# Kernel optimization log

Hardware: AMD Instinct MI355X
Metric: run time of the kernel (lower is better)

Reference implementation:

```python
import jax, jax.numpy as jnp
import numpy as np

AH, AW = 8, 8            # aligned_height, aligned_width
SCALE = 0.0625           # spatial_scale = 1/16
IMG = 1024               # image size implied by 64x64 feature map at stride 16


def setup_inputs() -> dict:
    key = jax.random.key(0)
    k1, k2, k3, k4, k5 = jax.random.split(key, 5)
    B, C, H, W = 4, 256, 64, 64
    N = 2000
    features = jax.random.normal(k1, (B, C, H, W), dtype=jnp.float32)
    # ROIs: (batch_idx, x1, y1, x2, y2) in image coordinates
    bidx = jax.random.randint(k2, (N,), 0, B).astype(jnp.float32)
    cx = jax.random.uniform(k3, (N,), minval=0.0, maxval=IMG)
    cy = jax.random.uniform(k4, (N,), minval=0.0, maxval=IMG)
    wh = jax.random.uniform(k5, (N, 2), minval=32.0, maxval=512.0)
    x1 = jnp.clip(cx - wh[:, 0] / 2, 0.0, IMG - 1.0)
    y1 = jnp.clip(cy - wh[:, 1] / 2, 0.0, IMG - 1.0)
    x2 = jnp.clip(cx + wh[:, 0] / 2, x1 + 16.0, float(IMG))
    y2 = jnp.clip(cy + wh[:, 1] / 2, y1 + 16.0, float(IMG))
    rois = jnp.stack([bidx, x1, y1, x2, y2], axis=1).astype(jnp.float32)
    return {"features": features, "rois": rois}


def _roi_align(features, rois):
    # Classic RoIAlign (crop_and_resize style): one bilinear sample per output
    # cell, sample grid spans the ROI with (aligned-1) intervals.
    B, C, H, W = features.shape
    N = rois.shape[0]
    b = rois[:, 0].astype(jnp.int32)
    x1 = rois[:, 1] * SCALE
    y1 = rois[:, 2] * SCALE
    x2 = rois[:, 3] * SCALE
    y2 = rois[:, 4] * SCALE
    bin_h = (y2 - y1) / (AH - 1.0)
    bin_w = (x2 - x1) / (AW - 1.0)
    ys = y1[:, None, None] + bin_h[:, None, None] * jnp.arange(AH, dtype=jnp.float32)[None, :, None]
    xs = x1[:, None, None] + bin_w[:, None, None] * jnp.arange(AW, dtype=jnp.float32)[None, None, :]
    ys = jnp.broadcast_to(ys, (N, AH, AW))
    xs = jnp.broadcast_to(xs, (N, AH, AW))
    valid = (ys >= 0) & (ys < H) & (xs >= 0) & (xs < W)
    y0 = jnp.floor(ys)
    x0 = jnp.floor(xs)
    ly = ys - y0  # bilinear weights
    lx = xs - x0
    iy0 = jnp.clip(y0.astype(jnp.int32), 0, H - 1)
    ix0 = jnp.clip(x0.astype(jnp.int32), 0, W - 1)
    iy1 = jnp.clip(iy0 + 1, 0, H - 1)
    ix1 = jnp.clip(ix0 + 1, 0, W - 1)
    bb = b[:, None, None]

    def g(iy, ix):
        return features[bb, :, iy, ix]  # [N, AH, AW, C]

    ly_ = ly[..., None]
    lx_ = lx[..., None]
    v = ((1 - ly_) * (1 - lx_) * g(iy0, ix0)
         + (1 - ly_) * lx_ * g(iy0, ix1)
         + ly_ * (1 - lx_) * g(iy1, ix0)
         + ly_ * lx_ * g(iy1, ix1))
    v = jnp.where(valid[..., None], v, 0.0)
    return jnp.transpose(v, (0, 3, 1, 2))  # [N, C, AH, AW]


def _max_pool_2x2_s1(x):
    # max_pool2d(kernel_size=2, stride=1): [N,C,h,w] -> [N,C,h-1,w-1]
    return jnp.maximum(
        jnp.maximum(x[:, :, :-1, :-1], x[:, :, :-1, 1:]),
        jnp.maximum(x[:, :, 1:, :-1], x[:, :, 1:, 1:]),
    )


def reference(features, rois):
    x = _roi_align(features, rois)
    return _max_pool_2x2_s1(x)  # [N, C, AH-1, AW-1]
```

## Files before the change

kernel.cpp:

```cpp
#include <hip/hip_runtime.h>
#include <cstdint>

constexpr int CCH = 256;
constexpr int HH  = 64;
constexpr int WW  = 64;
constexpr int OHW = 49;
constexpr float RSCALE = 0.0625f;

#define FMUL __fmul_rn
#define FADD __fadd_rn
#define FSUB __fsub_rn
#define FDIV __fdiv_rn

typedef float     v4f __attribute__((ext_vector_type(4)));
typedef _Float16  h2  __attribute__((ext_vector_type(2)));
typedef _Float16  h4  __attribute__((ext_vector_type(4)));

__device__ __forceinline__ h2 pkrtz(float a, float b) {
  auto t = __builtin_amdgcn_cvt_pkrtz(a, b);
  union { decltype(t) s; h2 d; } c; c.s = t; return c.d;
}
__device__ __forceinline__ h4 bcast4(float a) {
  h2 t = pkrtz(a, a);
  return __builtin_shufflevector(t, t, 0, 1, 0, 1);
}
__device__ __forceinline__ h4 u2h(uint2 u) {
  union { uint2 u; h4 h; } c; c.u = u; return c.h;
}
__device__ __forceinline__ h4 h4max(h4 a, h4 b) {
  return __builtin_elementwise_max(a, b);
}

__global__ __launch_bounds__(256) void ktrans_sched(const float* __restrict__ in,
                                                    unsigned short* __restrict__ out,
                                                    const float* __restrict__ rois,
                                                    int N, int slots, int do_sched,
                                                    int B, int* __restrict__ meta) {
  const int t = threadIdx.x;

  if ((int)blockIdx.z == B) {
    if (blockIdx.x != 0 || blockIdx.y != 0 || !do_sched) return;
    __shared__ int cnt[4], rnk[4], off[4], slack[4], excess[4];
    if (t < 4) { cnt[t] = 0; rnk[t] = 0; }
    __syncthreads();
    for (int i = t; i < N; i += 256) atomicAdd(&cnt[(int)rois[i * 5]], 1);
    __syncthreads();
    if (t == 0) {
      int o = 0, cs = 0, ce = 0;
      for (int p = 0; p < 4; ++p) {
        off[p] = o; o += cnt[p];
        slack[p]  = cs; if (slots - cnt[p] > 0) cs += slots - cnt[p];
        excess[p] = ce; if (cnt[p] - slots > 0) ce += cnt[p] - slots;
        meta[p] = cnt[p]; meta[4 + p] = off[p]; meta[8 + p] = slack[p];
      }
    }
    __syncthreads();
    int* perm = meta + 16;
    for (int i = t; i < N; i += 256) {
      const int b = (int)rois[i * 5];
      perm[off[b] + atomicAdd(&rnk[b], 1)] = i;
    }
    __syncthreads();
    int* extra = meta + 16 + N;
    for (int p = 0; p < 4; ++p) {
      const int ex = cnt[p] - slots;
      for (int e = t; e < ex; e += 256) extra[excess[p] + e] = perm[off[p] + slots + e];
    }
    return;
  }

  __shared__ float tile[64][65];
  const int b  = blockIdx.z;
  const int c0 = blockIdx.y * 64;
  const int s0 = blockIdx.x * 64;
  const float* inb = in + (size_t)b * CCH * (HH * WW);
  unsigned short* outb = out + (size_t)b * (HH * WW) * CCH;

  const int cl = t >> 4, sq = t & 15;
#pragma unroll
  for (int k = 0; k < 4; ++k) {
    const int c = cl + 16 * k;
    const v4f v = __builtin_nontemporal_load(
        (const v4f*)(inb + (size_t)(c0 + c) * (HH * WW) + s0 + 4 * sq));
    tile[c][4 * sq + 0] = v[0];
    tile[c][4 * sq + 1] = v[1];
    tile[c][4 * sq + 2] = v[2];
    tile[c][4 * sq + 3] = v[3];
  }
  __syncthreads();
  const int cq = t & 15, rl = t >> 4;
#pragma unroll
  for (int k = 0; k < 4; ++k) {
    const int r = rl + 16 * k;
    union { h2 h; unsigned u; } p0, p1;
    p0.h.x = (_Float16)tile[4 * cq + 0][r];
    p0.h.y = (_Float16)tile[4 * cq + 1][r];
    p1.h.x = (_Float16)tile[4 * cq + 2][r];
    p1.h.y = (_Float16)tile[4 * cq + 3][r];
    uint2 w; w.x = p0.u; w.y = p1.u;
    *(uint2*)(outb + (size_t)(s0 + r) * CCH + c0 + 4 * cq) = w;
  }
}

__global__ __launch_bounds__(256, 6) void roi_kernel11(const uint2* __restrict__ feat,
                                                       const float* __restrict__ rois,
                                                       const int* __restrict__ meta,
                                                       int N, int use_perm,
                                                       float* __restrict__ out) {
  __shared__ __attribute__((aligned(16))) h4       ldsA[OHW * 32];
  __shared__ __attribute__((aligned(16))) _Float16 ldsC[(CCH / 2) * OHW];
  const int i = blockIdx.x;
  const int t = threadIdx.x;
  const int g = t & 31;
  const int r = t >> 5;

  int n, half;
  if (use_perm) {
    const int p = (i & 7) >> 1;
    half        = i & 1;
    const int s = i >> 3;
    const int c_ = meta[p];
    const int o_ = meta[4 + p];
    const int sl = meta[8 + p];
    const int* perm  = meta + 16;
    const int* extra = meta + 16 + N;
    n = (s < c_) ? perm[o_ + s] : extra[sl + (s - c_)];
  } else {
    n = i >> 1; half = i & 1;
  }

  const float rb = rois[n * 5 + 0];
  const float x1 = FMUL(rois[n * 5 + 1], RSCALE);
  const float y1 = FMUL(rois[n * 5 + 2], RSCALE);
  const float x2 = FMUL(rois[n * 5 + 3], RSCALE);
  const float y2 = FMUL(rois[n * 5 + 4], RSCALE);
  const int   b  = (int)rb;
  const float bh = FDIV(FSUB(y2, y1), 7.0f);
  const float bw = FDIV(FSUB(x2, x1), 7.0f);

  int   xo0[8], xo1[8];
  float lx[8];
  bool  xv[8];
#pragma unroll
  for (int q = 0; q < 8; ++q) {
    const float xs = FADD(x1, FMUL(bw, (float)q));
    xv[q] = (xs >= 0.0f) && (xs < (float)WW);
    const float xf = floorf(xs);
    lx[q] = FSUB(xs, xf);
    int a = (int)xf;
    a = a < 0 ? 0 : (a > WW - 1 ? WW - 1 : a);
    xo0[q] = a * (CCH / 4);
    xo1[q] = ((a + 1 > WW - 1) ? WW - 1 : a + 1) * (CCH / 4);
  }

  const float ys = FADD(y1, FMUL(bh, (float)r));
  const bool  yv = (ys >= 0.0f) && (ys < (float)HH);
  const float yf = floorf(ys);
  const float ly = FSUB(ys, yf);
  int d = (int)yf;
  d = d < 0 ? 0 : (d > HH - 1 ? HH - 1 : d);
  const int d1 = (d + 1 > HH - 1) ? HH - 1 : d + 1;

  const uint2* fb = feat + (size_t)b * (HH * WW) * (CCH / 4) + (half * 32 + g);
  const uint2* r0 = fb + (size_t)d  * (WW * (CCH / 4));
  const uint2* r1 = fb + (size_t)d1 * (WW * (CCH / 4));
  const float wy1 = ly, wy0 = 1.0f - ly;

  h4 hc[7], vprev;
#pragma unroll
  for (int h = 0; h < 2; ++h) {
    uint2 g00[4], g01[4], g10[4], g11[4];
#pragma unroll
    for (int q = 0; q < 4; ++q) {
      const int s = 4 * h + q;
      g00[q] = r0[xo0[s]];
      g01[q] = r0[xo1[s]];
      g10[q] = r1[xo0[s]];
      g11[q] = r1[xo1[s]];
    }
    h4 v[4];
#pragma unroll
    for (int q = 0; q < 4; ++q) {
      const int s = 4 * h + q;
      const bool ok = yv && xv[s];
      const float wx1 = lx[s], wx0 = 1.0f - wx1;
      const h4 w00 = bcast4(wy0 * wx0);
      const h4 w01 = bcast4(wy0 * wx1);
      const h4 w10 = bcast4(wy1 * wx0);
      const h4 w11 = bcast4(wy1 * wx1);
      h4 rr = w00 * u2h(g00[q]) + w01 * u2h(g01[q])
            + w10 * u2h(g10[q]) + w11 * u2h(g11[q]);
      v[q] = ok ? rr : h4{};
    }
    if (h == 0) {
      hc[0] = h4max(v[0], v[1]);
      hc[1] = h4max(v[1], v[2]);
      hc[2] = h4max(v[2], v[3]);
      vprev = v[3];
    } else {
      hc[3] = h4max(vprev, v[0]);
      hc[4] = h4max(v[0], v[1]);
      hc[5] = h4max(v[1], v[2]);
      hc[6] = h4max(v[2], v[3]);
    }
  }

  if (r >= 1) {
#pragma unroll
    for (int m = 0; m < 7; ++m)
      ldsA[((r - 1) * 7 + m) * 32 + g] = hc[m];
  }
  __syncthreads();

  if (r <= 6) {
    _Float16* cb = ldsC + (4 * g) * OHW + r * 7;
#pragma unroll
    for (int m = 0; m < 7; ++m) {
      const h4 x = h4max(hc[m], ldsA[(r * 7 + m) * 32 + g]);
      cb[0 * OHW + m] = x[0];
      cb[1 * OHW + m] = x[1];
      cb[2 * OHW + m] = x[2];
      cb[3 * OHW + m] = x[3];
    }
  }
  __syncthreads();

  const uint2* cs = (const uint2*)ldsC;
  v4f* o4 = (v4f*)(out + (size_t)n * (CCH * OHW) + half * (CCH / 2) * OHW);
#pragma unroll
  for (int m = 0; m < 7; ++m) {
    const int idx = m * 256 + t;
    if (idx < (CCH / 2) * OHW / 4) {
      const uint2 qv = cs[idx];
      union { unsigned u; h2 h; } c0, c1;
      c0.u = qv.x; c1.u = qv.y;
      v4f wv;
      wv.x = (float)c0.h.x;
      wv.y = (float)c0.h.y;
      wv.z = (float)c1.h.x;
      wv.w = (float)c1.h.y;
      __builtin_nontemporal_store(wv, o4 + idx);
    }
  }
}

__global__ __launch_bounds__(256) void roi_kernel_fb(const float* __restrict__ feat,
                                                     const float* __restrict__ rois,
                                                     float* __restrict__ out) {
  __shared__ float sout[CCH * OHW];
  const int n = blockIdx.x;
  const int c = threadIdx.x;

  const float rb = rois[n * 5 + 0];
  const float x1 = FMUL(rois[n * 5 + 1], RSCALE);
  const float y1 = FMUL(rois[n * 5 + 2], RSCALE);
  const float x2 = FMUL(rois[n * 5 + 3], RSCALE);
  const float y2 = FMUL(rois[n * 5 + 4], RSCALE);
  const int b = (int)rb;
  const float bh = FDIV(FSUB(y2, y1), 7.0f);
  const float bw = FDIV(FSUB(x2, x1), 7.0f);

  int ix0[8], ix1[8], iy0[8], iy1[8];
  float lx[8], ly[8];
  bool xv[8], yv[8];
#pragma unroll
  for (int i = 0; i < 8; ++i) {
    const float xs = FADD(x1, FMUL(bw, (float)i));
    const float ys = FADD(y1, FMUL(bh, (float)i));
    xv[i] = (xs >= 0.0f) && (xs < (float)WW);
    yv[i] = (ys >= 0.0f) && (ys < (float)HH);
    const float xf = floorf(xs);
    const float yf = floorf(ys);
    lx[i] = FSUB(xs, xf);
    ly[i] = FSUB(ys, yf);
    int a = (int)xf;
    a = a < 0 ? 0 : (a > WW - 1 ? WW - 1 : a);
    ix0[i] = a;
    ix1[i] = (a + 1 > WW - 1) ? WW - 1 : a + 1;
    int d = (int)yf;
    d = d < 0 ? 0 : (d > HH - 1 ? HH - 1 : d);
    iy0[i] = d;
    iy1[i] = (d + 1 > HH - 1) ? HH - 1 : d + 1;
  }

  const float* fbp = feat + ((size_t)b * CCH + c) * (size_t)(HH * WW);
  float hp[7];
#pragma unroll
  for (int j = 0; j < 8; ++j) {
    float v[8];
    const float wy1 = ly[j], wy0 = 1.0f - ly[j];
#pragma unroll
    for (int i = 0; i < 8; ++i) {
      if (yv[j] && xv[i]) {
        const float f00 = fbp[iy0[j] * WW + ix0[i]];
        const float f01 = fbp[iy0[j] * WW + ix1[i]];
        const float f10 = fbp[iy1[j] * WW + ix0[i]];
        const float f11 = fbp[iy1[j] * WW + ix1[i]];
        const float wx1 = lx[i], wx0 = 1.0f - wx1;
        v[i] = wy0 * (wx0 * f00 + wx1 * f01) + wy1 * (wx0 * f10 + wx1 * f11);
      } else {
        v[i] = 0.0f;
      }
    }
    float hc[7];
#pragma unroll
    for (int i = 0; i < 7; ++i) hc[i] = fmaxf(v[i], v[i + 1]);
    if (j > 0) {
#pragma unroll
      for (int i = 0; i < 7; ++i)
        sout[c * OHW + (j - 1) * 7 + i] = fmaxf(hp[i], hc[i]);
    }
#pragma unroll
    for (int i = 0; i < 7; ++i) hp[i] = hc[i];
  }
  __syncthreads();
  const float4* s4 = (const float4*)sout;
  float4* o4 = (float4*)(out + (size_t)n * (CCH * OHW));
  for (int q = c; q < (CCH * OHW) / 4; q += 256) o4[q] = s4[q];
}

extern "C" void kernel_launch(void* const* d_in, const int* in_sizes, int n_in,
                              void* d_out, int out_size, void* d_ws, size_t ws_size,
                              hipStream_t stream) {
  (void)n_in; (void)out_size;
  const float* feat = (const float*)d_in[0];
  const float* rois = (const float*)d_in[1];
  float* out = (float*)d_out;
  const int N = in_sizes[1] / 5;
  const int B = in_sizes[0] / (CCH * HH * WW);
  const int M = 2 * N;
  const size_t featbf_bytes = (size_t)in_sizes[0] * sizeof(unsigned short);
  const size_t meta_bytes   = (size_t)(16 + 2 * N) * sizeof(int);

  if (ws_size >= featbf_bytes + meta_bytes) {
    unsigned short* featbf = (unsigned short*)d_ws;
    int* meta = (int*)((char*)d_ws + featbf_bytes);
    const int use_perm = (B == 4 && (M & 7) == 0) ? 1 : 0;

    ktrans_sched<<<dim3((HH * WW) / 64, CCH / 64, B + 1), dim3(256), 0, stream>>>(
        feat, featbf, rois, N, M >> 3, use_perm, B, meta);
    roi_kernel11<<<dim3(M), dim3(256), 0, stream>>>(
        (const uint2*)featbf, rois, meta, N, use_perm, out);
  } else {
    roi_kernel_fb<<<dim3(N), dim3(256), 0, stream>>>(feat, rois, out);
  }
}
```

Measured before the change: 130.5 us.

## Use persistent grid-stride blocks and issue all 32 gathers before blending

The ROI kernel becomes a persistent grid-stride loop capped at 2048 blocks, and the per-partition meta values are hoisted into registers once per block. All 32 bilinear gather loads for the eight x samples are now issued up front instead of in two batches of 16, to raise memory-level parallelism. The occupancy hint drops from 6 to 4 waves per SIMD to make room for the extra live registers. The catch is lower occupancy, and because work is interleaved by grid stride, the block-to-ROI assignment no longer follows the original launch order.

```diff
diff --git a/kernel.cpp b/kernel.cpp
--- a/kernel.cpp
+++ b/kernel.cpp
@@ -102,144 +102,154 @@
   }
 }
 
-__global__ __launch_bounds__(256, 6) void roi_kernel11(const uint2* __restrict__ feat,
+__global__ __launch_bounds__(256, 4) void roi_kernel12(const uint2* __restrict__ feat,
                                                        const float* __restrict__ rois,
                                                        const int* __restrict__ meta,
-                                                       int N, int use_perm,
+                                                       int N, int M, int use_perm,
                                                        float* __restrict__ out) {
   __shared__ __attribute__((aligned(16))) h4       ldsA[OHW * 32];
   __shared__ __attribute__((aligned(16))) _Float16 ldsC[(CCH / 2) * OHW];
-  const int i = blockIdx.x;
   const int t = threadIdx.x;
   const int g = t & 31;
   const int r = t >> 5;
 
-  int n, half;
-  if (use_perm) {
-    const int p = (i & 7) >> 1;
-    half        = i & 1;
-    const int s = i >> 3;
-    const int c_ = meta[p];
-    const int o_ = meta[4 + p];
-    const int sl = meta[8 + p];
-    const int* perm  = meta + 16;
-    const int* extra = meta + 16 + N;
-    n = (s < c_) ? perm[o_ + s] : extra[sl + (s - c_)];
-  } else {
-    n = i >> 1; half = i & 1;
-  }
-
-  const float rb = rois[n * 5 + 0];
-  const float x1 = FMUL(rois[n * 5 + 1], RSCALE);
-  const float y1 = FMUL(rois[n * 5 + 2], RSCALE);
-  const float x2 = FMUL(rois[n * 5 + 3], RSCALE);
-  const float y2 = FMUL(rois[n * 5 + 4], RSCALE);
-  const int   b  = (int)rb;
-  const float bh = FDIV(FSUB(y2, y1), 7.0f);
-  const float bw = FDIV(FSUB(x2, x1), 7.0f);
-
-  int   xo0[8], xo1[8];
-  float lx[8];
-  bool  xv[8];
-#pragma unroll
-  for (int q = 0; q < 8; ++q) {
-    const float xs = FADD(x1, FMUL(bw, (float)q));
-    xv[q] = (xs >= 0.0f) && (xs < (float)WW);
-    const float xf = floorf(xs);
-    lx[q] = FSUB(xs, xf);
-    int a = (int)xf;
-    a = a < 0 ? 0 : (a > WW - 1 ? WW - 1 : a);
-    xo0[q] = a * (CCH / 4);
-    xo1[q] = ((a + 1 > WW - 1) ? WW - 1 : a + 1) * (CCH / 4);
-  }
-
-  const float ys = FADD(y1, FMUL(bh, (float)r));
-  const bool  yv = (ys >= 0.0f) && (ys < (float)HH);
-  const float yf = floorf(ys);
-  const float ly = FSUB(ys, yf);
-  int d = (int)yf;
-  d = d < 0 ? 0 : (d > HH - 1 ? HH - 1 : d);
-  const int d1 = (d + 1 > HH - 1) ? HH - 1 : d + 1;
-
-  const uint2* fb = feat + (size_t)b * (HH * WW) * (CCH / 4) + (half * 32 + g);
-  const uint2* r0 = fb + (size_t)d  * (WW * (CCH / 4));
-  const uint2* r1 = fb + (size_t)d1 * (WW * (CCH / 4));
-  const float wy1 = ly, wy0 = 1.0f - ly;
-
-  h4 hc[7], vprev;
-#pragma unroll
-  for (int h = 0; h < 2; ++h) {
-    uint2 g00[4], g01[4], g10[4], g11[4];
-#pragma unroll
-    for (int q = 0; q < 4; ++q) {
-      const int s = 4 * h + q;
-      g00[q] = r0[xo0[s]];
-      g01[q] = r0[xo1[s]];
-      g10[q] = r1[xo0[s]];
-      g11[q] = r1[xo1[s]];
-    }
-    h4 v[4];
-#pragma unroll
-    for (int q = 0; q < 4; ++q) {
-      const int s = 4 * h + q;
-      const bool ok = yv && xv[s];
-      const float wx1 = lx[s], wx0 = 1.0f - wx1;
-      const h4 w00 = bcast4(wy0 * wx0);
-      const h4 w01 = bcast4(wy0 * wx1);
-      const h4 w10 = bcast4(wy1 * wx0);
-      const h4 w11 = bcast4(wy1 * wx1);
-      h4 rr = w00 * u2h(g00[q]) + w01 * u2h(g01[q])
-            + w10 * u2h(g10[q]) + w11 * u2h(g11[q]);
-      v[q] = ok ? rr : h4{};
-    }
-    if (h == 0) {
-      hc[0] = h4max(v[0], v[1]);
-      hc[1] = h4max(v[1], v[2]);
-      hc[2] = h4max(v[2], v[3]);
-      vprev = v[3];
+  const int c0_ = use_perm ? meta[0] : 0;
+  const int c1_ = use_perm ? meta[1] : 0;
+  const int c2_ = use_perm ? meta[2] : 0;
+  const int c3_ = use_perm ? meta[3] : 0;
+  const int o0_ = use_perm ? meta[4] : 0, o1_ = use_perm ? meta[5] : 0;
+  const int o2_ = use_perm ? meta[6] : 0, o3_ = use_perm ? meta[7] : 0;
+  const int s0_ = use_perm ? meta[8] : 0, s1_ = use_perm ? meta[9] : 0;
+  const int s2_ = use_perm ? meta[10] : 0, s3_ = use_perm ? meta[11] : 0;
+  const int* perm  = meta + 16;
+  const int* extra = meta + 16 + N;
+
+  for (int i = blockIdx.x; i < M; i += gridDim.x) {
+    int n, half;
+    if (use_perm) {
+      const int p = (i & 7) >> 1;
+      half        = i & 1;
+      const int s = i >> 3;
+      const int c_ = p == 0 ? c0_ : (p == 1 ? c1_ : (p == 2 ? c2_ : c3_));
+      const int o_ = p == 0 ? o0_ : (p == 1 ? o1_ : (p == 2 ? o2_ : o3_));
+      const int sl = p == 0 ? s0_ : (p == 1 ? s1_ : (p == 2 ? s2_ : s3_));
+      n = (s < c_) ? perm[o_ + s] : extra[sl + (s - c_)];
     } else {
-      hc[3] = h4max(vprev, v[0]);
-      hc[4] = h4max(v[0], v[1]);
-      hc[5] = h4max(v[1], v[2]);
-      hc[6] = h4max(v[2], v[3]);
-    }
-  }
-
-  if (r >= 1) {
-#pragma unroll
-    for (int m = 0; m < 7; ++m)
-      ldsA[((r - 1) * 7 + m) * 32 + g] = hc[m];
-  }
-  __syncthreads();
-
-  if (r <= 6) {
-    _Float16* cb = ldsC + (4 * g) * OHW + r * 7;
+      n = i >> 1; half = i & 1;
+    }
+
+    const float rb = rois[n * 5 + 0];
+    const float x1 = FMUL(rois[n * 5 + 1], RSCALE);
+    const float y1 = FMUL(rois[n * 5 + 2], RSCALE);
+    const float x2 = FMUL(rois[n * 5 + 3], RSCALE);
+    const float y2 = FMUL(rois[n * 5 + 4], RSCALE);
+    const int   b  = (int)rb;
+    const float bh = FDIV(FSUB(y2, y1), 7.0f);
+    const float bw = FDIV(FSUB(x2, x1), 7.0f);
+
+    int   xo0[8], xo1[8];
+    float lx[8];
+    bool  xv[8];
+#pragma unroll
+    for (int q = 0; q < 8; ++q) {
+      const float xs = FADD(x1, FMUL(bw, (float)q));
+      xv[q] = (xs >= 0.0f) && (xs < (float)WW);
+      const float xf = floorf(xs);
+      lx[q] = FSUB(xs, xf);
+      int a = (int)xf;
+      a = a < 0 ? 0 : (a > WW - 1 ? WW - 1 : a);
+      xo0[q] = a * (CCH / 4);
+      xo1[q] = ((a + 1 > WW - 1) ? WW - 1 : a + 1) * (CCH / 4);
+    }
+
+    const float ys = FADD(y1, FMUL(bh, (float)r));
+    const bool  yv = (ys >= 0.0f) && (ys < (float)HH);
+    const float yf = floorf(ys);
+    const float ly = FSUB(ys, yf);
+    int d = (int)yf;
+    d = d < 0 ? 0 : (d > HH - 1 ? HH - 1 : d);
+    const int d1 = (d + 1 > HH - 1) ? HH - 1 : d + 1;
+
+    const uint2* fb = feat + (size_t)b * (HH * WW) * (CCH / 4) + (half * 32 + g);
+    const uint2* r0 = fb + (size_t)d  * (WW * (CCH / 4));
+    const uint2* r1 = fb + (size_t)d1 * (WW * (CCH / 4));
+    const float wy1 = ly, wy0 = 1.0f - ly;
+
+    uint2 g00[8], g01[8], g10[8], g11[8];
+#pragma unroll
+    for (int q = 0; q < 8; ++q) {
+      g00[q] = r0[xo0[q]];
+      g01[q] = r0[xo1[q]];
+      g10[q] = r1[xo0[q]];
+      g11[q] = r1[xo1[q]];
+    }
+
+    h4 hc[7], vprev;
+#pragma unroll
+    for (int h = 0; h < 2; ++h) {
+      h4 v[4];
+#pragma unroll
+      for (int q = 0; q < 4; ++q) {
+        const int s = 4 * h + q;
+        const bool ok = yv && xv[s];
+        const float wx1 = lx[s], wx0 = 1.0f - wx1;
+        const h4 w00 = bcast4(wy0 * wx0);
+        const h4 w01 = bcast4(wy0 * wx1);
+        const h4 w10 = bcast4(wy1 * wx0);
+        const h4 w11 = bcast4(wy1 * wx1);
+        h4 rr = w00 * u2h(g00[s]) + w01 * u2h(g01[s])
+              + w10 * u2h(g10[s]) + w11 * u2h(g11[s]);
+        v[q] = ok ? rr : h4{};
+      }
+      if (h == 0) {
+        hc[0] = h4max(v[0], v[1]);
+        hc[1] = h4max(v[1], v[2]);
+        hc[2] = h4max(v[2], v[3]);
+        vprev = v[3];
+      } else {
+        hc[3] = h4max(vprev, v[0]);
+        hc[4] = h4max(v[0], v[1]);
+        hc[5] = h4max(v[1], v[2]);
+        hc[6] = h4max(v[2], v[3]);
+      }
+    }
+
+    if (r >= 1) {
+#pragma unroll
+      for (int m = 0; m < 7; ++m)
+        ldsA[((r - 1) * 7 + m) * 32 + g] = hc[m];
+    }
+    __syncthreads();
+
+    if (r <= 6) {
+      _Float16* cb = ldsC + (4 * g) * OHW + r * 7;
+#pragma unroll
+      for (int m = 0; m < 7; ++m) {
+        const h4 x = h4max(hc[m], ldsA[(r * 7 + m) * 32 + g]);
+        cb[0 * OHW + m] = x[0];
+        cb[1 * OHW + m] = x[1];
+        cb[2 * OHW + m] = x[2];
+        cb[3 * OHW + m] = x[3];
+      }
+    }
+    __syncthreads();
+
+    const uint2* cs = (const uint2*)ldsC;
+    v4f* o4 = (v4f*)(out + (size_t)n * (CCH * OHW) + half * (CCH / 2) * OHW);
 #pragma unroll
     for (int m = 0; m < 7; ++m) {
-      const h4 x = h4max(hc[m], ldsA[(r * 7 + m) * 32 + g]);
-      cb[0 * OHW + m] = x[0];
-      cb[1 * OHW + m] = x[1];
-      cb[2 * OHW + m] = x[2];
-      cb[3 * OHW + m] = x[3];
-    }
-  }
-  __syncthreads();
-
-  const uint2* cs = (const uint2*)ldsC;
-  v4f* o4 = (v4f*)(out + (size_t)n * (CCH * OHW) + half * (CCH / 2) * OHW);
-#pragma unroll
-  for (int m = 0; m < 7; ++m) {
-    const int idx = m * 256 + t;
-    if (idx < (CCH / 2) * OHW / 4) {
-      const uint2 qv = cs[idx];
-      union { unsigned u; h2 h; } c0, c1;
-      c0.u = qv.x; c1.u = qv.y;
-      v4f wv;
-      wv.x = (float)c0.h.x;
-      wv.y = (float)c0.h.y;
-      wv.z = (float)c1.h.x;
-      wv.w = (float)c1.h.y;
-      __builtin_nontemporal_store(wv, o4 + idx);
+      const int idx = m * 256 + t;
+      if (idx < (CCH / 2) * OHW / 4) {
+        const uint2 qv = cs[idx];
+        union { unsigned u; h2 h; } e0, e1;
+        e0.u = qv.x; e1.u = qv.y;
+        v4f wv;
+        wv.x = (float)e0.h.x;
+        wv.y = (float)e0.h.y;
+        wv.z = (float)e1.h.x;
+        wv.w = (float)e1.h.y;
+        __builtin_nontemporal_store(wv, o4 + idx);
+      }
     }
   }
 }
@@ -339,8 +349,9 @@
 
     ktrans_sched<<<dim3((HH * WW) / 64, CCH / 64, B + 1), dim3(256), 0, stream>>>(
         feat, featbf, rois, N, M >> 3, use_perm, B, meta);
-    roi_kernel11<<<dim3(M), dim3(256), 0, stream>>>(
-        (const uint2*)featbf, rois, meta, N, use_perm, out);
+    const int grid = (M >= 2048) ? 2048 : M;
+    roi_kernel12<<<dim3(grid), dim3(256), 0, stream>>>(
+        (const uint2*)featbf, rois, meta, N, M, use_perm, out);
   } else {
     roi_kernel_fb<<<dim3(N), dim3(256), 0, stream>>>(feat, rois, out);
   }
```

After: 133.1 us. Within noise of the previous version (+2.0%).

## Process both channel halves of an ROI in one 512-thread block

Applied to the files above, without the earlier changes.

The ROI kernel now launches one 512-thread block per ROI instead of two 256-thread blocks, each handling half the channels. The two halves share the ROI coordinate setup and the scheduling lookup, and the output is written as one contiguous store per ROI. The scheduling slot mapping is changed to match the halved block count. LDS use per block doubles, which may reduce how many blocks fit on each CU.

```diff
diff --git a/kernel.cpp b/kernel.cpp
--- a/kernel.cpp
+++ b/kernel.cpp
@@ -102,23 +102,24 @@
   }
 }
 
-__global__ __launch_bounds__(256, 6) void roi_kernel11(const uint2* __restrict__ feat,
+__global__ __launch_bounds__(512, 6) void roi_kernel16(const uint2* __restrict__ feat,
                                                        const float* __restrict__ rois,
                                                        const int* __restrict__ meta,
                                                        int N, int use_perm,
                                                        float* __restrict__ out) {
-  __shared__ __attribute__((aligned(16))) h4       ldsA[OHW * 32];
-  __shared__ __attribute__((aligned(16))) _Float16 ldsC[(CCH / 2) * OHW];
-  const int i = blockIdx.x;
-  const int t = threadIdx.x;
-  const int g = t & 31;
-  const int r = t >> 5;
-
-  int n, half;
+  __shared__ __attribute__((aligned(16))) h4       ldsA[OHW * 64];
+  __shared__ __attribute__((aligned(16))) _Float16 ldsC[CCH * OHW];
+  const int i  = blockIdx.x;
+  const int t  = threadIdx.x;
+  const int half = t >> 8;
+  const int tt = t & 255;
+  const int g  = tt & 31;
+  const int r  = tt >> 5;
+
+  int n;
   if (use_perm) {
     const int p = (i & 7) >> 1;
-    half        = i & 1;
-    const int s = i >> 3;
+    const int s = ((i >> 3) << 1) | (i & 1);
     const int c_ = meta[p];
     const int o_ = meta[4 + p];
     const int sl = meta[8 + p];
@@ -126,7 +127,7 @@
     const int* extra = meta + 16 + N;
     n = (s < c_) ? perm[o_ + s] : extra[sl + (s - c_)];
   } else {
-    n = i >> 1; half = i & 1;
+    n = i;
   }
 
   const float rb = rois[n * 5 + 0];
@@ -208,15 +209,15 @@
   if (r >= 1) {
 #pragma unroll
     for (int m = 0; m < 7; ++m)
-      ldsA[((r - 1) * 7 + m) * 32 + g] = hc[m];
+      ldsA[((r - 1) * 7 + m) * 64 + half * 32 + g] = hc[m];
   }
   __syncthreads();
 
   if (r <= 6) {
-    _Float16* cb = ldsC + (4 * g) * OHW + r * 7;
+    _Float16* cb = ldsC + (half * 128 + 4 * g) * OHW + r * 7;
 #pragma unroll
     for (int m = 0; m < 7; ++m) {
-      const h4 x = h4max(hc[m], ldsA[(r * 7 + m) * 32 + g]);
+      const h4 x = h4max(hc[m], ldsA[(r * 7 + m) * 64 + half * 32 + g]);
       cb[0 * OHW + m] = x[0];
       cb[1 * OHW + m] = x[1];
       cb[2 * OHW + m] = x[2];
@@ -226,19 +227,19 @@
   __syncthreads();
 
   const uint2* cs = (const uint2*)ldsC;
-  v4f* o4 = (v4f*)(out + (size_t)n * (CCH * OHW) + half * (CCH / 2) * OHW);
+  v4f* o4 = (v4f*)(out + (size_t)n * (CCH * OHW));
 #pragma unroll
   for (int m = 0; m < 7; ++m) {
-    const int idx = m * 256 + t;
-    if (idx < (CCH / 2) * OHW / 4) {
+    const int idx = m * 512 + t;
+    if (m < 6 || t < 64) {
       const uint2 qv = cs[idx];
-      union { unsigned u; h2 h; } c0, c1;
-      c0.u = qv.x; c1.u = qv.y;
+      union { unsigned u; h2 h; } e0, e1;
+      e0.u = qv.x; e1.u = qv.y;
       v4f wv;
-      wv.x = (float)c0.h.x;
-      wv.y = (float)c0.h.y;
-      wv.z = (float)c1.h.x;
-      wv.w = (float)c1.h.y;
+      wv.x = (float)e0.h.x;
+      wv.y = (float)e0.h.y;
+      wv.z = (float)e1.h.x;
+      wv.w = (float)e1.h.y;
       __builtin_nontemporal_store(wv, o4 + idx);
     }
   }
@@ -328,18 +329,18 @@
   float* out = (float*)d_out;
   const int N = in_sizes[1] / 5;
   const int B = in_sizes[0] / (CCH * HH * WW);
-  const int M = 2 * N;
   const size_t featbf_bytes = (size_t)in_sizes[0] * sizeof(unsigned short);
   const size_t meta_bytes   = (size_t)(16 + 2 * N) * sizeof(int);
 
   if (ws_size >= featbf_bytes + meta_bytes) {
     unsigned short* featbf = (unsigned short*)d_ws;
     int* meta = (int*)((char*)d_ws + featbf_bytes);
-    const int use_perm = (B == 4 && (M & 7) == 0) ? 1 : 0;
+    const int use_perm = (B == 4 && (N & 7) == 0) ? 1 : 0;
+    const int slots = N >> 2;
 
     ktrans_sched<<<dim3((HH * WW) / 64, CCH / 64, B + 1), dim3(256), 0, stream>>>(
-        feat, featbf, rois, N, M >> 3, use_perm, B, meta);
-    roi_kernel11<<<dim3(M), dim3(256), 0, stream>>>(
+        feat, featbf, rois, N, slots, use_perm, B, meta);
+    roi_kernel16<<<dim3(N), dim3(512), 0, stream>>>(
         (const uint2*)featbf, rois, meta, N, use_perm, out);
   } else {
     roi_kernel_fb<<<dim3(N), dim3(256), 0, stream>>>(feat, rois, out);
```

Measured after the change: 134.2 us. 2.8% more time.
